# Performance work log

Measured on AMD Instinct MI355X. Metric: run time of the kernel, lower is better.

The kernel has to match this reference:

```python
import jax, jax.numpy as jnp
import numpy as np

N = 50000        # nodes
E = 1600000      # edges (before self-loops)
HID = 128
HEADS = 4
HD = HID // HEADS
FIN = 32 + 7     # node feats + scenario feats
EPS = 1e-5


def _ln(x, g, b):
    m = x.mean(-1, keepdims=True)
    v = ((x - m) ** 2).mean(-1, keepdims=True)
    return (x - m) / jnp.sqrt(v + EPS) * g + b


def _gat(x, src, dst, W, a_s, a_d, bias):
    # PyG GATConv (concat=True, negative_slope=0.2), eval mode (no dropout)
    xp = (x @ W).reshape(-1, HEADS, HD)                    # [N,H,C]
    es = (xp * a_s).sum(-1)                                # [N,H]
    ed = (xp * a_d).sum(-1)                                # [N,H]
    e = jax.nn.leaky_relu(es[src] + ed[dst], 0.2)          # [Etot,H]
    emax = jax.ops.segment_max(e, dst, num_segments=N)     # per-target softmax (self-loops guarantee nonempty segments)
    a = jnp.exp(e - emax[dst])
    denom = jax.ops.segment_sum(a, dst, num_segments=N)
    a = a / denom[dst]
    out = jax.ops.segment_sum(xp[src] * a[:, :, None], dst, num_segments=N)
    return out.reshape(-1, HID) + bias


def setup_inputs() -> dict:
    key = jax.random.key(0)
    ks = iter(jax.random.split(key, 64))

    def rn(shape, scale=0.05):
        return jax.random.normal(next(ks), shape, dtype=jnp.float32) * scale

    inp = {}
    inp["x"] = jax.random.normal(next(ks), (N, FIN), dtype=jnp.float32)
    inp["edge_index"] = jax.random.randint(next(ks), (2, E), 0, N)
    inp["enc_w1"] = rn((FIN, HID)); inp["enc_b1"] = jnp.zeros((HID,), jnp.float32)
    inp["enc_w2"] = rn((HID, HID)); inp["enc_b2"] = jnp.zeros((HID,), jnp.float32)
    for l in (1, 2, 3):
        inp[f"W{l}"] = rn((HID, HID))
        inp[f"as{l}"] = rn((HEADS, HD))
        inp[f"ad{l}"] = rn((HEADS, HD))
        inp[f"bc{l}"] = jnp.zeros((HID,), jnp.float32)
        inp[f"g{l}"] = jnp.ones((HID,), jnp.float32)
        inp[f"be{l}"] = jnp.zeros((HID,), jnp.float32)
    inp["imp_w1"] = rn((HID, HID // 2)); inp["imp_b1"] = jnp.zeros((HID // 2,), jnp.float32)
    inp["imp_w2"] = rn((HID // 2, 3));   inp["imp_b2"] = jnp.zeros((3,), jnp.float32)
    inp["tim_w1"] = rn((HID, HID // 2)); inp["tim_b1"] = jnp.zeros((HID // 2,), jnp.float32)
    inp["tim_w2"] = rn((HID // 2, 2));   inp["tim_b2"] = jnp.zeros((2,), jnp.float32)
    return inp


def reference(x, edge_index, enc_w1, enc_b1, enc_w2, enc_b2,
              W1, as1, ad1, bc1, g1, be1,
              W2, as2, ad2, bc2, g2, be2,
              W3, as3, ad3, bc3, g3, be3,
              imp_w1, imp_b1, imp_w2, imp_b2,
              tim_w1, tim_b1, tim_w2, tim_b2):
    loops = jnp.arange(N, dtype=edge_index.dtype)          # add_self_loops=True
    src = jnp.concatenate([edge_index[0], loops])
    dst = jnp.concatenate([edge_index[1], loops])
    h = jax.nn.relu(x @ enc_w1 + enc_b1) @ enc_w2 + enc_b2
    for (W, a_s, a_d, bc, g, be) in ((W1, as1, ad1, bc1, g1, be1),
                                     (W2, as2, ad2, bc2, g2, be2),
                                     (W3, as3, ad3, bc3, g3, be3)):
        h = jax.nn.relu(_ln(_gat(h, src, dst, W, a_s, a_d, bc) + h, g, be))
    impact = jax.nn.relu(h @ imp_w1 + imp_b1) @ imp_w2 + imp_b2
    timing = jax.nn.softplus(jax.nn.relu(h @ tim_w1 + tim_b1) @ tim_w2 + tim_b2)
    return (impact, timing)
```

## Files before the change

### kernel.cpp

```cpp
#include <hip/hip_runtime.h>
#include <hip/hip_bf16.h>
#include <math.h>

#define NN 50000
#define EDGES 1600000
#define ETOT (EDGES + NN)
#define FINDIM 39
#define NPART 256
#define PSZ 196
#define PCAP 7100
#define P1TILE 4096

__device__ __forceinline__ unsigned pack_bf16(float a, float b) {
    __hip_bfloat162 t;
    t.x = __float2bfloat16(a);
    t.y = __float2bfloat16(b);
    return *(unsigned*)&t;
}
__device__ __forceinline__ float2 unpack_bf16(unsigned w) {
    float2 r;
    r.x = __uint_as_float(w << 16);
    r.y = __uint_as_float(w & 0xffff0000u);
    return r;
}

__device__ __forceinline__ int src_at(const int* ei, int i, bool i32) {
    return i32 ? ei[i] : ei[2 * i];
}
__device__ __forceinline__ int dst_at(const int* ei, int i, bool i32) {
    return i32 ? ei[EDGES + i] : ei[2 * (EDGES + i)];
}

__global__ __launch_bounds__(256) void pass1_kernel(const int* __restrict__ ei,
                                                    int* __restrict__ gcursor,
                                                    unsigned* __restrict__ pbuf) {
    __shared__ unsigned raw[P1TILE];
    __shared__ unsigned srt[P1TILE];
    __shared__ int pcnt[NPART], poff[NPART], pcur[NPART], gb[NPART];
    __shared__ int i32flag;
    int t = threadIdx.x;
    if (t == 0) i32flag = 0;
    __syncthreads();
    int chunk = (ETOT + gridDim.x - 1) / gridDim.x;
    int c0 = blockIdx.x * chunk;
    int c1 = c0 + chunk; if (c1 > ETOT) c1 = ETOT;
    int sb = c0 < EDGES - 64 ? c0 : 0;
    if (t < 64 && ei[2 * (sb + t) + 1] != 0) i32flag = 1;
    __syncthreads();
    bool i32 = (i32flag != 0);
    for (int t0 = c0; t0 < c1; t0 += P1TILE) {
        int tn = c1 - t0; if (tn > P1TILE) tn = P1TILE;
        pcnt[t] = 0; pcur[t] = 0;
        __syncthreads();
        for (int i = t; i < tn; i += 256) {
            int e = t0 + i;
            int s, d;
            if (e < EDGES) { s = src_at(ei, e, i32); d = dst_at(ei, e, i32); }
            else { s = d = e - EDGES; }
            raw[i] = ((unsigned)s << 16) | (unsigned)d;
            atomicAdd(&pcnt[d / PSZ], 1);
        }
        __syncthreads();
        poff[t] = pcnt[t];
        __syncthreads();
        for (int off = 1; off < NPART; off <<= 1) {
            int v = (t >= off) ? poff[t - off] : 0;
            __syncthreads();
            poff[t] += v;
            __syncthreads();
        }
        poff[t] -= pcnt[t];
        gb[t] = atomicAdd(&gcursor[t], pcnt[t]);
        __syncthreads();
        for (int i = t; i < tn; i += 256) {
            unsigned r = raw[i];
            int part = (int)(r & 0xFFFFu) / PSZ;
            int pos = poff[part] + atomicAdd(&pcur[part], 1);
            srt[pos] = r;
        }
        __syncthreads();
        for (int i = t; i < tn; i += 256) {
            unsigned r = srt[i];
            int part = (int)(r & 0xFFFFu) / PSZ;
            int gpos = gb[part] + (i - poff[part]);
            if (gpos < PCAP) pbuf[(size_t)part * PCAP + gpos] = r;
        }
        __syncthreads();
    }
}

__global__ __launch_bounds__(256) void pass2_kernel(const unsigned* __restrict__ pbuf,
                                                    const int* __restrict__ gcursor,
                                                    int* __restrict__ rowptr,
                                                    int* __restrict__ colidx) {
    __shared__ unsigned recs[PCAP];
    __shared__ int lhist[PSZ], lexcl[PSZ], lcur[PSZ];
    __shared__ int psm[NPART];
    int p = blockIdx.x;
    int t = threadIdx.x;
    psm[t] = gcursor[t];
    __syncthreads();
    for (int off = 1; off < NPART; off <<= 1) {
        int x = (t >= off) ? psm[t - off] : 0;
        __syncthreads();
        psm[t] += x;
        __syncthreads();
    }
    int n = gcursor[p]; if (n > PCAP) n = PCAP;
    int base = psm[p] - gcursor[p];
    if (p == NPART - 1 && t == 0) rowptr[NN] = psm[NPART - 1];
    int d0 = p * PSZ;
    int nd = NN - d0; if (nd > PSZ) nd = PSZ;
    if (nd < 0) nd = 0;
    for (int i = t; i < nd; i += 256) { lhist[i] = 0; lcur[i] = 0; }
    __syncthreads();
    for (int i = t; i < n; i += 256) {
        unsigned r = pbuf[(size_t)p * PCAP + i];
        recs[i] = r;
        atomicAdd(&lhist[(int)(r & 0xFFFFu) - d0], 1);
    }
    __syncthreads();
    for (int i = t; i < nd; i += 256) lexcl[i] = lhist[i];
    __syncthreads();
    for (int off = 1; off < PSZ; off <<= 1) {
        int a0 = 0;
        if (t < nd && t >= off) a0 = lexcl[t - off];
        __syncthreads();
        if (t < nd) lexcl[t] += a0;
        __syncthreads();
    }
    for (int i = t; i < nd; i += 256) {
        lexcl[i] -= lhist[i];
        rowptr[d0 + i] = base + lexcl[i];
    }
    __syncthreads();
    for (int i = t; i < n; i += 256) {
        unsigned r = recs[i];
        int li = (int)(r & 0xFFFFu) - d0;
        int pos = base + lexcl[li] + atomicAdd(&lcur[li], 1);
        colidx[pos] = (int)(r >> 16);
    }
}

template <int NC, bool RELU>
__global__ __launch_bounds__(256) void gemm_small_kernel(const float* __restrict__ A,
                                                         const float* __restrict__ B,
                                                         const float* __restrict__ bias,
                                                         float* __restrict__ C, int M, int K) {
    constexpr int TM = 32;
    constexpr int GROUPS = 256 / NC;
    constexpr int RPG = TM / GROUPS;
    constexpr int KC = 64;
    __shared__ float As[TM * 128];
    __shared__ float Bs[KC * NC];
    int t = threadIdx.x;
    int i0 = blockIdx.x * TM;

    int rows = M - i0; if (rows > TM) rows = TM;
    for (int idx = t; idx < rows * K; idx += 256) {
        int r = idx / K, k = idx - r * K;
        As[r * K + k] = A[(size_t)(i0 + r) * K + k];
    }

    int col = t % NC, grp = t / NC;
    int rg0 = grp * RPG;
    float acc[RPG];
#pragma unroll
    for (int r = 0; r < RPG; ++r) acc[r] = 0.f;

    for (int k0 = 0; k0 < K; k0 += KC) {
        int kc = K - k0; if (kc > KC) kc = KC;
        __syncthreads();
        for (int idx = t; idx < kc * NC; idx += 256) Bs[idx] = B[(size_t)k0 * NC + idx];
        __syncthreads();
        for (int k = 0; k < kc; ++k) {
            float bv = Bs[k * NC + col];
#pragma unroll
            for (int r = 0; r < RPG; ++r) acc[r] += As[(rg0 + r) * K + k0 + k] * bv;
        }
    }

    float bb = bias ? bias[col] : 0.f;
#pragma unroll
    for (int r = 0; r < RPG; ++r) {
        int i = i0 + rg0 + r;
        if (i < M) {
            float v = acc[r] + bb;
            if (RELU) v = v > 0.f ? v : 0.f;
            C[(size_t)i * NC + col] = v;
        }
    }
}

template <bool BIAS, bool EPI>
__global__ __launch_bounds__(256) void gemm128_kernel(const float* __restrict__ A,
                                                      const float* __restrict__ B,
                                                      const float* __restrict__ bias,
                                                      float* __restrict__ C,
                                                      unsigned* __restrict__ XP,
                                                      const float* __restrict__ a_s,
                                                      const float* __restrict__ a_d,
                                                      float* __restrict__ es,
                                                      float* __restrict__ ed, int M) {
    __shared__ float As[64 * 32];
    __shared__ float Bs[32 * 128];
    int t = threadIdx.x;
    int i0 = blockIdx.x * 64;
    int tc = t & 31;
    int tr = t >> 5;
    int r0 = tr * 8;
    int c0 = tc * 4;

    float acc[8][4];
#pragma unroll
    for (int i = 0; i < 8; ++i)
#pragma unroll
        for (int j = 0; j < 4; ++j) acc[i][j] = 0.f;

    for (int k0 = 0; k0 < 128; k0 += 32) {
        __syncthreads();
#pragma unroll
        for (int q = 0; q < 2; ++q) {
            int idx = t + q * 256;
            int r = idx >> 3, kq = idx & 7;
            float4 v4 = make_float4(0.f, 0.f, 0.f, 0.f);
            if (i0 + r < M) v4 = *(const float4*)&A[(size_t)(i0 + r) * 128 + k0 + kq * 4];
            *(float4*)&As[r * 32 + kq * 4] = v4;
        }
#pragma unroll
        for (int q = 0; q < 4; ++q) {
            int idx = (t + q * 256) * 4;
            *(float4*)&Bs[idx] = *(const float4*)&B[(size_t)k0 * 128 + idx];
        }
        __syncthreads();
#pragma unroll 8
        for (int k = 0; k < 32; k += 4) {
            float4 a4[8];
#pragma unroll
            for (int i = 0; i < 8; ++i)
                a4[i] = *(const float4*)&As[(r0 + i) * 32 + k];
            float4 b4[4];
#pragma unroll
            for (int kk = 0; kk < 4; ++kk)
                b4[kk] = *(const float4*)&Bs[(k + kk) * 128 + c0];
#pragma unroll
            for (int i = 0; i < 8; ++i) {
                const float* av = (const float*)&a4[i];
#pragma unroll
                for (int kk = 0; kk < 4; ++kk) {
                    acc[i][0] += av[kk] * b4[kk].x;
                    acc[i][1] += av[kk] * b4[kk].y;
                    acc[i][2] += av[kk] * b4[kk].z;
                    acc[i][3] += av[kk] * b4[kk].w;
                }
            }
        }
    }

    if (!EPI) {
        float4 bias4 = make_float4(0.f, 0.f, 0.f, 0.f);
        if (BIAS) bias4 = *(const float4*)&bias[c0];
#pragma unroll
        for (int i = 0; i < 8; ++i) {
            int row = i0 + r0 + i;
            if (row < M) {
                float4 o;
                o.x = acc[i][0] + bias4.x;
                o.y = acc[i][1] + bias4.y;
                o.z = acc[i][2] + bias4.z;
                o.w = acc[i][3] + bias4.w;
                *(float4*)&C[(size_t)row * 128 + c0] = o;
            }
        }
    } else {
#pragma unroll
        for (int i = 0; i < 8; ++i) {
            int row = i0 + r0 + i;
            if (row < M) {
                uint2 o;
                o.x = pack_bf16(acc[i][0], acc[i][1]);
                o.y = pack_bf16(acc[i][2], acc[i][3]);
                *(uint2*)&XP[(size_t)row * 64 + tc * 2] = o;
            }
        }
        int hd = tc >> 3;
        float4 s4 = *(const float4*)&a_s[c0];
        float4 d4 = *(const float4*)&a_d[c0];
#pragma unroll
        for (int i = 0; i < 8; ++i) {
            int row = i0 + r0 + i;
            float s = acc[i][0] * s4.x + acc[i][1] * s4.y + acc[i][2] * s4.z + acc[i][3] * s4.w;
            float d = acc[i][0] * d4.x + acc[i][1] * d4.y + acc[i][2] * d4.z + acc[i][3] * d4.w;
#pragma unroll
            for (int off = 4; off >= 1; off >>= 1) {
                s += __shfl_xor(s, off);
                d += __shfl_xor(d, off);
            }
            if ((tc & 7) == 0 && row < M) {
                es[row * 4 + hd] = s;
                ed[row * 4 + hd] = d;
            }
        }
    }
}

__global__ __launch_bounds__(256) void gemm_heads_kernel(const float* __restrict__ A,
                                                         const float* __restrict__ iw1,
                                                         const float* __restrict__ ib1,
                                                         const float* __restrict__ tw1,
                                                         const float* __restrict__ tb1,
                                                         const float* __restrict__ iw2,
                                                         const float* __restrict__ ib2,
                                                         const float* __restrict__ tw2,
                                                         const float* __restrict__ tb2,
                                                         float* __restrict__ out, int M) {
    __shared__ float As[64 * 32];
    __shared__ float Bs[32 * 128];
    int t = threadIdx.x;
    int i0 = blockIdx.x * 64;
    int tc = t & 31;
    int tr = t >> 5;
    int r0 = tr * 8;
    int c0 = tc * 4;

    float acc[8][4];
#pragma unroll
    for (int i = 0; i < 8; ++i)
#pragma unroll
        for (int j = 0; j < 4; ++j) acc[i][j] = 0.f;

    for (int k0 = 0; k0 < 128; k0 += 32) {
        __syncthreads();
#pragma unroll
        for (int q = 0; q < 2; ++q) {
            int idx = t + q * 256;
            int r = idx >> 3, kq = idx & 7;
            float4 v4 = make_float4(0.f, 0.f, 0.f, 0.f);
            if (i0 + r < M) v4 = *(const float4*)&A[(size_t)(i0 + r) * 128 + k0 + kq * 4];
            *(float4*)&As[r * 32 + kq * 4] = v4;
        }
#pragma unroll
        for (int q = 0; q < 4; ++q) {
            int idx = (t + q * 256) * 4;
            int k = idx >> 7, cl = idx & 127;
            float4 v4 = (cl < 64)
                ? *(const float4*)&iw1[(size_t)(k0 + k) * 64 + cl]
                : *(const float4*)&tw1[(size_t)(k0 + k) * 64 + (cl - 64)];
            *(float4*)&Bs[idx] = v4;
        }
        __syncthreads();
#pragma unroll 8
        for (int k = 0; k < 32; k += 4) {
            float4 a4[8];
#pragma unroll
            for (int i = 0; i < 8; ++i)
                a4[i] = *(const float4*)&As[(r0 + i) * 32 + k];
            float4 b4[4];
#pragma unroll
            for (int kk = 0; kk < 4; ++kk)
                b4[kk] = *(const float4*)&Bs[(k + kk) * 128 + c0];
#pragma unroll
            for (int i = 0; i < 8; ++i) {
                const float* av = (const float*)&a4[i];
#pragma unroll
                for (int kk = 0; kk < 4; ++kk) {
                    acc[i][0] += av[kk] * b4[kk].x;
                    acc[i][1] += av[kk] * b4[kk].y;
                    acc[i][2] += av[kk] * b4[kk].z;
                    acc[i][3] += av[kk] * b4[kk].w;
                }
            }
        }
    }

    bool isimp = (tc < 16);
    int lc = isimp ? c0 : (c0 - 64);
    float v[8][4];
#pragma unroll
    for (int i = 0; i < 8; ++i)
#pragma unroll
        for (int j = 0; j < 4; ++j) {
            float b = isimp ? ib1[lc + j] : tb1[lc + j];
            float x = acc[i][j] + b;
            v[i][j] = x > 0.f ? x : 0.f;
        }
#pragma unroll
    for (int i = 0; i < 8; ++i) {
        int row = i0 + r0 + i;
        if (isimp) {
#pragma unroll
            for (int c = 0; c < 3; ++c) {
                float pc = v[i][0] * iw2[(lc + 0) * 3 + c] + v[i][1] * iw2[(lc + 1) * 3 + c]
                         + v[i][2] * iw2[(lc + 2) * 3 + c] + v[i][3] * iw2[(lc + 3) * 3 + c];
#pragma unroll
                for (int off = 8; off >= 1; off >>= 1) pc += __shfl_xor(pc, off);
                if (tc == 0 && row < M) out[(size_t)row * 3 + c] = pc + ib2[c];
            }
        } else {
#pragma unroll
            for (int d = 0; d < 2; ++d) {
                float pd = v[i][0] * tw2[(lc + 0) * 2 + d] + v[i][1] * tw2[(lc + 1) * 2 + d]
                         + v[i][2] * tw2[(lc + 2) * 2 + d] + v[i][3] * tw2[(lc + 3) * 2 + d];
#pragma unroll
                for (int off = 8; off >= 1; off >>= 1) pd += __shfl_xor(pd, off);
                if (tc == 16 && row < M) {
                    float a = pd + tb2[d];
                    float sp = a > 20.f ? a : log1pf(__expf(a));
                    out[(size_t)(NN * 3) + (size_t)row * 2 + d] = sp;
                }
            }
        }
    }
}

__global__ __launch_bounds__(256, 6) void gat_kernel(const unsigned* __restrict__ xpk,
                                                     const float* __restrict__ es,
                                                     const float* __restrict__ ed,
                                                     const int* __restrict__ rowptr,
                                                     const int* __restrict__ colidx,
                                                     float* __restrict__ h,
                                                     const float* __restrict__ bc,
                                                     const float* __restrict__ g,
                                                     const float* __restrict__ be) {
    int wv = threadIdx.x >> 6, l = threadIdx.x & 63;
    int hf = l >> 5;
    int lh = l & 31;
    int hd = lh >> 3;
    int j  = lh & 7;
    int v = blockIdx.x * 8 + wv * 2 + hf;
    if (v >= NN) return;
    int s0 = rowptr[v], s1 = rowptr[v + 1];
    int len = s1 - s0;
    int nmax = max(len, __shfl_xor(len, 32));
    int c0 = (hd << 5) + (j << 2);
    int xsel = (hd << 4) + (j << 1);
    float edv = ed[((unsigned)v << 2) + hd];

    float4 h4 = *(const float4*)&h[(size_t)v * 128 + c0];

    float a0 = 0.f, a1 = 0.f, a2 = 0.f, a3 = 0.f, den = 0.f;
    for (int p8 = 0; p8 < nmax; p8 += 8) {
        int u[8];
#pragma unroll
        for (int q = 0; q < 8; ++q) {
            int idx = p8 + q;
            u[q] = colidx[s0 + (idx < len ? idx : len - 1)];
        }
        uint2 xw[8];
#pragma unroll
        for (int q = 0; q < 8; ++q)
            xw[q] = *(const uint2*)&xpk[((unsigned)u[q] << 6) + xsel];
        float w[8];
#pragma unroll
        for (int q = 0; q < 8; ++q) {
            float e = es[((unsigned)u[q] << 2) + hd] + edv;
            e = fmaxf(e, 0.2f * e);
            float ww = __expf(e);
            w[q] = (p8 + q < len) ? ww : 0.f;
            den += w[q];
        }
#pragma unroll
        for (int q = 0; q < 8; ++q) {
            float2 x0 = unpack_bf16(xw[q].x);
            float2 x1 = unpack_bf16(xw[q].y);
            a0 = fmaf(w[q], x0.x, a0);
            a1 = fmaf(w[q], x0.y, a1);
            a2 = fmaf(w[q], x1.x, a2);
            a3 = fmaf(w[q], x1.y, a3);
        }
    }
    float rd = 1.f / den;

    float4 bc4 = *(const float4*)&bc[c0];
    float y0 = a0 * rd + bc4.x + h4.x;
    float y1 = a1 * rd + bc4.y + h4.y;
    float y2 = a2 * rd + bc4.z + h4.z;
    float y3 = a3 * rd + bc4.w + h4.w;

    float s = y0 + y1 + y2 + y3;
#pragma unroll
    for (int off = 16; off >= 1; off >>= 1) s += __shfl_xor(s, off);
    float mean = s * (1.f / 128.f);
    float d0 = y0 - mean, d1 = y1 - mean, d2 = y2 - mean, d3 = y3 - mean;
    float vv = d0 * d0 + d1 * d1 + d2 * d2 + d3 * d3;
#pragma unroll
    for (int off = 16; off >= 1; off >>= 1) vv += __shfl_xor(vv, off);
    float rstd = rsqrtf(vv * (1.f / 128.f) + 1e-5f);
    float4 g4  = *(const float4*)&g[c0];
    float4 be4 = *(const float4*)&be[c0];
    float z0 = d0 * rstd * g4.x + be4.x;
    float z1 = d1 * rstd * g4.y + be4.y;
    float z2 = d2 * rstd * g4.z + be4.z;
    float z3 = d3 * rstd * g4.w + be4.w;
    float4 o;
    o.x = z0 > 0.f ? z0 : 0.f;
    o.y = z1 > 0.f ? z1 : 0.f;
    o.z = z2 > 0.f ? z2 : 0.f;
    o.w = z3 > 0.f ? z3 : 0.f;
    *(float4*)&h[(size_t)v * 128 + c0] = o;
}

extern "C" void kernel_launch(void* const* d_in, const int* in_sizes, int n_in,
                              void* d_out, int out_size, void* d_ws, size_t ws_size,
                              hipStream_t stream) {
    const float* x      = (const float*)d_in[0];
    const int*   ei     = (const int*)d_in[1];
    const float* enc_w1 = (const float*)d_in[2];
    const float* enc_b1 = (const float*)d_in[3];
    const float* enc_w2 = (const float*)d_in[4];
    const float* enc_b2 = (const float*)d_in[5];
    const float *W[3], *as_[3], *ad_[3], *bc[3], *g[3], *be[3];
    for (int l = 0; l < 3; ++l) {
        W[l]   = (const float*)d_in[6 + l * 6 + 0];
        as_[l] = (const float*)d_in[6 + l * 6 + 1];
        ad_[l] = (const float*)d_in[6 + l * 6 + 2];
        bc[l]  = (const float*)d_in[6 + l * 6 + 3];
        g[l]   = (const float*)d_in[6 + l * 6 + 4];
        be[l]  = (const float*)d_in[6 + l * 6 + 5];
    }
    const float* imp_w1 = (const float*)d_in[24];
    const float* imp_b1 = (const float*)d_in[25];
    const float* imp_w2 = (const float*)d_in[26];
    const float* imp_b2 = (const float*)d_in[27];
    const float* tim_w1 = (const float*)d_in[28];
    const float* tim_b1 = (const float*)d_in[29];
    const float* tim_w2 = (const float*)d_in[30];
    const float* tim_b2 = (const float*)d_in[31];

    int* gcursor = (int*)d_ws;
    int* rowptr  = gcursor + NPART + 64;
    int* colidx  = rowptr + NN + 1;
    uintptr_t pb = (uintptr_t)(colidx + ETOT + 8);
    pb = (pb + 255) & ~(uintptr_t)255;
    unsigned* pbuf = (unsigned*)pb;
    uintptr_t fb = (uintptr_t)(pbuf + (size_t)NPART * PCAP);
    fb = (fb + 255) & ~(uintptr_t)255;
    float* es = (float*)fb;
    float* ed = es + (size_t)NN * 4;
    float* h  = ed + (size_t)NN * 4;
    float* xpf = h + (size_t)NN * 128;
    unsigned* xpk = (unsigned*)xpf;
    float* tmp = xpf;

    hipMemsetAsync(gcursor, 0, NPART * sizeof(int), stream);
    pass1_kernel<<<512, 256, 0, stream>>>(ei, gcursor, pbuf);
    pass2_kernel<<<NPART, 256, 0, stream>>>(pbuf, gcursor, rowptr, colidx);

    const int GB64 = (NN + 63) / 64;
    gemm_small_kernel<128, true><<<(NN + 31) / 32, 256, 0, stream>>>(x, enc_w1, enc_b1, tmp, NN, FINDIM);
    gemm128_kernel<true, false><<<GB64, 256, 0, stream>>>(tmp, enc_w2, enc_b2, h, nullptr,
                                                          nullptr, nullptr, nullptr, nullptr, NN);

    for (int l = 0; l < 3; ++l) {
        gemm128_kernel<false, true><<<GB64, 256, 0, stream>>>(h, W[l], nullptr, nullptr, xpk,
                                                              as_[l], ad_[l], es, ed, NN);
        gat_kernel<<<(NN + 7) / 8, 256, 0, stream>>>(xpk, es, ed, rowptr, colidx, h,
                                                     bc[l], g[l], be[l]);
    }

    gemm_heads_kernel<<<GB64, 256, 0, stream>>>(h, imp_w1, imp_b1, tim_w1, tim_b1,
                                                imp_w2, imp_b2, tim_w2, tim_b2,
                                                (float*)d_out, NN);
}
```

Baseline: 562.5 us.

## Precompute exponentials per node and use 16-lane-per-node GAT aggregation

The projection GEMM now stores exp(s), exp(0.2s), exp(d) and exp(0.2d) per node and head. The GAT kernel then forms each edge weight as the max of two products, which equals exp(leaky_relu(s+d)), so there is no per-edge exp. The GAT kernel also assigns 16 lanes per node instead of 32, with each lane gathering 8 bf16 features via uint4 loads, and it lowers the occupancy hint to 5. Dropping the max subtraction in the softmax risks overflow for large logits, and the per-node es/ed arrays double in size.

```diff
diff --git a/kernel.cpp b/kernel.cpp
--- a/kernel.cpp
+++ b/kernel.cpp
@@ -200,8 +200,8 @@
                                                       unsigned* __restrict__ XP,
                                                       const float* __restrict__ a_s,
                                                       const float* __restrict__ a_d,
-                                                      float* __restrict__ es,
-                                                      float* __restrict__ ed, int M) {
+                                                      float* __restrict__ esx,
+                                                      float* __restrict__ edx, int M) {
     __shared__ float As[64 * 32];
     __shared__ float Bs[32 * 128];
     int t = threadIdx.x;
@@ -297,8 +297,11 @@
                 d += __shfl_xor(d, off);
             }
             if ((tc & 7) == 0 && row < M) {
-                es[row * 4 + hd] = s;
-                ed[row * 4 + hd] = d;
+                float2 E, F;
+                E.x = __expf(s); E.y = __expf(0.2f * s);
+                F.x = __expf(d); F.y = __expf(0.2f * d);
+                *(float2*)&esx[row * 8 + hd * 2] = E;
+                *(float2*)&edx[row * 8 + hd * 2] = F;
             }
         }
     }
@@ -413,9 +416,9 @@
     }
 }
 
-__global__ __launch_bounds__(256, 6) void gat_kernel(const unsigned* __restrict__ xpk,
-                                                     const float* __restrict__ es,
-                                                     const float* __restrict__ ed,
+__global__ __launch_bounds__(256, 5) void gat_kernel(const unsigned* __restrict__ xpk,
+                                                     const float* __restrict__ esx,
+                                                     const float* __restrict__ edx,
                                                      const int* __restrict__ rowptr,
                                                      const int* __restrict__ colidx,
                                                      float* __restrict__ h,
@@ -423,22 +426,26 @@
                                                      const float* __restrict__ g,
                                                      const float* __restrict__ be) {
     int wv = threadIdx.x >> 6, l = threadIdx.x & 63;
-    int hf = l >> 5;
-    int lh = l & 31;
-    int hd = lh >> 3;
-    int j  = lh & 7;
-    int v = blockIdx.x * 8 + wv * 2 + hf;
+    int qt = l >> 4;
+    int lq = l & 15;
+    int hd = lq >> 2;
+    int j  = lq & 3;
+    int v = blockIdx.x * 16 + wv * 4 + qt;
     if (v >= NN) return;
     int s0 = rowptr[v], s1 = rowptr[v + 1];
     int len = s1 - s0;
-    int nmax = max(len, __shfl_xor(len, 32));
-    int c0 = (hd << 5) + (j << 2);
-    int xsel = (hd << 4) + (j << 1);
-    float edv = ed[((unsigned)v << 2) + hd];
-
-    float4 h4 = *(const float4*)&h[(size_t)v * 128 + c0];
-
-    float a0 = 0.f, a1 = 0.f, a2 = 0.f, a3 = 0.f, den = 0.f;
+    int m1 = max(len, __shfl_xor(len, 16));
+    int nmax = max(m1, __shfl_xor(m1, 32));
+    int c0 = (hd << 5) + (j << 3);
+    int xsel = (hd << 4) + (j << 2);
+    float2 F = *(const float2*)&edx[((unsigned)v << 3) + (hd << 1)];
+
+    float4 h4a = *(const float4*)&h[(size_t)v * 128 + c0];
+    float4 h4b = *(const float4*)&h[(size_t)v * 128 + c0 + 4];
+
+    float a0 = 0.f, a1 = 0.f, a2 = 0.f, a3 = 0.f;
+    float a4 = 0.f, a5 = 0.f, a6 = 0.f, a7 = 0.f;
+    float den = 0.f;
     for (int p8 = 0; p8 < nmax; p8 += 8) {
         int u[8];
 #pragma unroll
@@ -446,16 +453,18 @@
             int idx = p8 + q;
             u[q] = colidx[s0 + (idx < len ? idx : len - 1)];
         }
-        uint2 xw[8];
+        float2 E[8];
 #pragma unroll
         for (int q = 0; q < 8; ++q)
-            xw[q] = *(const uint2*)&xpk[((unsigned)u[q] << 6) + xsel];
+            E[q] = *(const float2*)&esx[((unsigned)u[q] << 3) + (hd << 1)];
+        uint4 xw[8];
+#pragma unroll
+        for (int q = 0; q < 8; ++q)
+            xw[q] = *(const uint4*)&xpk[((unsigned)u[q] << 6) + xsel];
         float w[8];
 #pragma unroll
         for (int q = 0; q < 8; ++q) {
-            float e = es[((unsigned)u[q] << 2) + hd] + edv;
-            e = fmaxf(e, 0.2f * e);
-            float ww = __expf(e);
+            float ww = fmaxf(E[q].x * F.x, E[q].y * F.y);
             w[q] = (p8 + q < len) ? ww : 0.f;
             den += w[q];
         }
@@ -463,41 +472,58 @@
         for (int q = 0; q < 8; ++q) {
             float2 x0 = unpack_bf16(xw[q].x);
             float2 x1 = unpack_bf16(xw[q].y);
+            float2 x2 = unpack_bf16(xw[q].z);
+            float2 x3 = unpack_bf16(xw[q].w);
             a0 = fmaf(w[q], x0.x, a0);
             a1 = fmaf(w[q], x0.y, a1);
             a2 = fmaf(w[q], x1.x, a2);
             a3 = fmaf(w[q], x1.y, a3);
+            a4 = fmaf(w[q], x2.x, a4);
+            a5 = fmaf(w[q], x2.y, a5);
+            a6 = fmaf(w[q], x3.x, a6);
+            a7 = fmaf(w[q], x3.y, a7);
         }
     }
     float rd = 1.f / den;
 
-    float4 bc4 = *(const float4*)&bc[c0];
-    float y0 = a0 * rd + bc4.x + h4.x;
-    float y1 = a1 * rd + bc4.y + h4.y;
-    float y2 = a2 * rd + bc4.z + h4.z;
-    float y3 = a3 * rd + bc4.w + h4.w;
-
-    float s = y0 + y1 + y2 + y3;
-#pragma unroll
-    for (int off = 16; off >= 1; off >>= 1) s += __shfl_xor(s, off);
+    float4 bc4a = *(const float4*)&bc[c0];
+    float4 bc4b = *(const float4*)&bc[c0 + 4];
+    float y0 = a0 * rd + bc4a.x + h4a.x;
+    float y1 = a1 * rd + bc4a.y + h4a.y;
+    float y2 = a2 * rd + bc4a.z + h4a.z;
+    float y3 = a3 * rd + bc4a.w + h4a.w;
+    float y4 = a4 * rd + bc4b.x + h4b.x;
+    float y5 = a5 * rd + bc4b.y + h4b.y;
+    float y6 = a6 * rd + bc4b.z + h4b.z;
+    float y7 = a7 * rd + bc4b.w + h4b.w;
+
+    float s = ((y0 + y1) + (y2 + y3)) + ((y4 + y5) + (y6 + y7));
+#pragma unroll
+    for (int off = 8; off >= 1; off >>= 1) s += __shfl_xor(s, off);
     float mean = s * (1.f / 128.f);
     float d0 = y0 - mean, d1 = y1 - mean, d2 = y2 - mean, d3 = y3 - mean;
-    float vv = d0 * d0 + d1 * d1 + d2 * d2 + d3 * d3;
-#pragma unroll
-    for (int off = 16; off >= 1; off >>= 1) vv += __shfl_xor(vv, off);
+    float d4 = y4 - mean, d5 = y5 - mean, d6 = y6 - mean, d7 = y7 - mean;
+    float vv = ((d0 * d0 + d1 * d1) + (d2 * d2 + d3 * d3))
+             + ((d4 * d4 + d5 * d5) + (d6 * d6 + d7 * d7));
+#pragma unroll
+    for (int off = 8; off >= 1; off >>= 1) vv += __shfl_xor(vv, off);
     float rstd = rsqrtf(vv * (1.f / 128.f) + 1e-5f);
-    float4 g4  = *(const float4*)&g[c0];
-    float4 be4 = *(const float4*)&be[c0];
-    float z0 = d0 * rstd * g4.x + be4.x;
-    float z1 = d1 * rstd * g4.y + be4.y;
-    float z2 = d2 * rstd * g4.z + be4.z;
-    float z3 = d3 * rstd * g4.w + be4.w;
-    float4 o;
-    o.x = z0 > 0.f ? z0 : 0.f;
-    o.y = z1 > 0.f ? z1 : 0.f;
-    o.z = z2 > 0.f ? z2 : 0.f;
-    o.w = z3 > 0.f ? z3 : 0.f;
-    *(float4*)&h[(size_t)v * 128 + c0] = o;
+    float4 g4a  = *(const float4*)&g[c0];
+    float4 g4b  = *(const float4*)&g[c0 + 4];
+    float4 be4a = *(const float4*)&be[c0];
+    float4 be4b = *(const float4*)&be[c0 + 4];
+    float4 oa, ob;
+    float z;
+    z = d0 * rstd * g4a.x + be4a.x; oa.x = z > 0.f ? z : 0.f;
+    z = d1 * rstd * g4a.y + be4a.y; oa.y = z > 0.f ? z : 0.f;
+    z = d2 * rstd * g4a.z + be4a.z; oa.z = z > 0.f ? z : 0.f;
+    z = d3 * rstd * g4a.w + be4a.w; oa.w = z > 0.f ? z : 0.f;
+    z = d4 * rstd * g4b.x + be4b.x; ob.x = z > 0.f ? z : 0.f;
+    z = d5 * rstd * g4b.y + be4b.y; ob.y = z > 0.f ? z : 0.f;
+    z = d6 * rstd * g4b.z + be4b.z; ob.z = z > 0.f ? z : 0.f;
+    z = d7 * rstd * g4b.w + be4b.w; ob.w = z > 0.f ? z : 0.f;
+    *(float4*)&h[(size_t)v * 128 + c0] = oa;
+    *(float4*)&h[(size_t)v * 128 + c0 + 4] = ob;
 }
 
 extern "C" void kernel_launch(void* const* d_in, const int* in_sizes, int n_in,
@@ -535,9 +561,9 @@
     unsigned* pbuf = (unsigned*)pb;
     uintptr_t fb = (uintptr_t)(pbuf + (size_t)NPART * PCAP);
     fb = (fb + 255) & ~(uintptr_t)255;
-    float* es = (float*)fb;
-    float* ed = es + (size_t)NN * 4;
-    float* h  = ed + (size_t)NN * 4;
+    float* esx = (float*)fb;
+    float* edx = esx + (size_t)NN * 8;
+    float* h   = edx + (size_t)NN * 8;
     float* xpf = h + (size_t)NN * 128;
     unsigned* xpk = (unsigned*)xpf;
     float* tmp = xpf;
@@ -553,9 +579,9 @@
 
     for (int l = 0; l < 3; ++l) {
         gemm128_kernel<false, true><<<GB64, 256, 0, stream>>>(h, W[l], nullptr, nullptr, xpk,
-                                                              as_[l], ad_[l], es, ed, NN);
-        gat_kernel<<<(NN + 7) / 8, 256, 0, stream>>>(xpk, es, ed, rowptr, colidx, h,
-                                                     bc[l], g[l], be[l]);
+                                                              as_[l], ad_[l], esx, edx, NN);
+        gat_kernel<<<(NN + 15) / 16, 256, 0, stream>>>(xpk, esx, edx, rowptr, colidx, h,
+                                                       bc[l], g[l], be[l]);
     }
 
     gemm_heads_kernel<<<GB64, 256, 0, stream>>>(h, imp_w1, imp_b1, tim_w1, tim_b1,
```

Measured after the change: 584.6 us. +3.9%, slower.

## Use bf16 MFMA for GAT projections and precompute exponentials of attention logits

Applied to the files above, without the earlier changes.

Replaces the fp32 FMA GEMM for each GAT layer's projection with a bf16 MFMA kernel. It reads a bf16 copy of h, written by the encoder GEMM and the previous GAT layer, and a transposed bf16 copy of W. The attention epilogue now stores exp(s) and exp(0.2s) per node, so the per-edge leaky-relu+exp becomes a max of two products. This cuts the per-edge transcendental work and the GEMM cost. In exchange it reads more per-edge bytes (float2 instead of float), adds bf16 rounding on the GEMM inputs, and risks overflow from the unshifted exponentials.

```diff
diff --git a/kernel.cpp b/kernel.cpp
--- a/kernel.cpp
+++ b/kernel.cpp
@@ -10,6 +10,9 @@
 #define PSZ 196
 #define PCAP 7100
 #define P1TILE 4096
+
+typedef __attribute__((ext_vector_type(8))) short short8;
+typedef __attribute__((ext_vector_type(4))) float floatx4;
 
 __device__ __forceinline__ unsigned pack_bf16(float a, float b) {
     __hip_bfloat162 t;
@@ -192,16 +195,11 @@
     }
 }
 
-template <bool BIAS, bool EPI>
 __global__ __launch_bounds__(256) void gemm128_kernel(const float* __restrict__ A,
                                                       const float* __restrict__ B,
                                                       const float* __restrict__ bias,
                                                       float* __restrict__ C,
-                                                      unsigned* __restrict__ XP,
-                                                      const float* __restrict__ a_s,
-                                                      const float* __restrict__ a_d,
-                                                      float* __restrict__ es,
-                                                      float* __restrict__ ed, int M) {
+                                                      unsigned* __restrict__ HB, int M) {
     __shared__ float As[64 * 32];
     __shared__ float Bs[32 * 128];
     int t = threadIdx.x;
@@ -257,48 +255,115 @@
         }
     }
 
-    if (!EPI) {
-        float4 bias4 = make_float4(0.f, 0.f, 0.f, 0.f);
-        if (BIAS) bias4 = *(const float4*)&bias[c0];
-#pragma unroll
-        for (int i = 0; i < 8; ++i) {
-            int row = i0 + r0 + i;
-            if (row < M) {
-                float4 o;
-                o.x = acc[i][0] + bias4.x;
-                o.y = acc[i][1] + bias4.y;
-                o.z = acc[i][2] + bias4.z;
-                o.w = acc[i][3] + bias4.w;
-                *(float4*)&C[(size_t)row * 128 + c0] = o;
-            }
-        }
-    } else {
-#pragma unroll
-        for (int i = 0; i < 8; ++i) {
-            int row = i0 + r0 + i;
-            if (row < M) {
-                uint2 o;
-                o.x = pack_bf16(acc[i][0], acc[i][1]);
-                o.y = pack_bf16(acc[i][2], acc[i][3]);
-                *(uint2*)&XP[(size_t)row * 64 + tc * 2] = o;
-            }
-        }
-        int hd = tc >> 3;
-        float4 s4 = *(const float4*)&a_s[c0];
-        float4 d4 = *(const float4*)&a_d[c0];
-#pragma unroll
-        for (int i = 0; i < 8; ++i) {
-            int row = i0 + r0 + i;
-            float s = acc[i][0] * s4.x + acc[i][1] * s4.y + acc[i][2] * s4.z + acc[i][3] * s4.w;
-            float d = acc[i][0] * d4.x + acc[i][1] * d4.y + acc[i][2] * d4.z + acc[i][3] * d4.w;
-#pragma unroll
-            for (int off = 4; off >= 1; off >>= 1) {
+    float4 bias4 = *(const float4*)&bias[c0];
+#pragma unroll
+    for (int i = 0; i < 8; ++i) {
+        int row = i0 + r0 + i;
+        if (row < M) {
+            float4 o;
+            o.x = acc[i][0] + bias4.x;
+            o.y = acc[i][1] + bias4.y;
+            o.z = acc[i][2] + bias4.z;
+            o.w = acc[i][3] + bias4.w;
+            *(float4*)&C[(size_t)row * 128 + c0] = o;
+            uint2 p;
+            p.x = pack_bf16(o.x, o.y);
+            p.y = pack_bf16(o.z, o.w);
+            *(uint2*)&HB[(size_t)row * 64 + tc * 2] = p;
+        }
+    }
+}
+
+__global__ __launch_bounds__(256) void wconv_kernel(const float* __restrict__ W,
+                                                    unsigned short* __restrict__ wtb) {
+    int idx = blockIdx.x * 256 + threadIdx.x;
+    int c = idx >> 7, k = idx & 127;
+    unsigned p = pack_bf16(W[(size_t)k * 128 + c], 0.f);
+    wtb[(size_t)c * 128 + k] = (unsigned short)(p & 0xffffu);
+}
+
+__global__ __launch_bounds__(256) void gemm_mfma_kernel(const unsigned* __restrict__ hb,
+                                                        const unsigned short* __restrict__ wtb,
+                                                        unsigned* __restrict__ XP,
+                                                        const float* __restrict__ a_s,
+                                                        const float* __restrict__ a_d,
+                                                        float* __restrict__ esx,
+                                                        float* __restrict__ edx, int M) {
+    int t = threadIdx.x;
+    int w = t >> 6, l = t & 63;
+    int c = l & 15, grp = l >> 4;
+    int i0 = blockIdx.x * 64 + w * 16;
+    int arow = i0 + c;
+
+    floatx4 acc[8];
+#pragma unroll
+    for (int n = 0; n < 8; ++n) acc[n] = (floatx4){0.f, 0.f, 0.f, 0.f};
+
+    uint4 a4[4];
+#pragma unroll
+    for (int kc = 0; kc < 4; ++kc) {
+        uint4 z = make_uint4(0u, 0u, 0u, 0u);
+        if (arow < M) z = *(const uint4*)&hb[(size_t)arow * 64 + (kc << 4) + (grp << 2)];
+        a4[kc] = z;
+    }
+
+#pragma unroll
+    for (int kc = 0; kc < 4; ++kc) {
+        short8 af = *(short8*)&a4[kc];
+#pragma unroll
+        for (int n = 0; n < 8; ++n) {
+            short8 bf = *(const short8*)&wtb[(size_t)(((n << 4) + c) * 128 + (kc << 5) + (grp << 3))];
+            acc[n] = __builtin_amdgcn_mfma_f32_16x16x32_bf16(af, bf, acc[n], 0, 0, 0);
+        }
+    }
+
+    float asv[8], adv[8];
+#pragma unroll
+    for (int n = 0; n < 8; ++n) { asv[n] = a_s[(n << 4) + c]; adv[n] = a_d[(n << 4) + c]; }
+
+    float sp[4][4], dp[4][4];
+#pragma unroll
+    for (int r = 0; r < 4; ++r)
+#pragma unroll
+        for (int hd = 0; hd < 4; ++hd) { sp[r][hd] = 0.f; dp[r][hd] = 0.f; }
+
+#pragma unroll
+    for (int n = 0; n < 8; ++n) {
+#pragma unroll
+        for (int r = 0; r < 4; ++r) {
+            float vv = acc[n][r];
+            float pv = __shfl_xor(vv, 1);
+            int row = i0 + (grp << 2) + r;
+            if (!(c & 1) && row < M)
+                XP[(size_t)row * 64 + (n << 3) + (c >> 1)] = pack_bf16(vv, pv);
+            sp[r][n >> 1] = fmaf(vv, asv[n], sp[r][n >> 1]);
+            dp[r][n >> 1] = fmaf(vv, adv[n], dp[r][n >> 1]);
+        }
+    }
+#pragma unroll
+    for (int r = 0; r < 4; ++r)
+#pragma unroll
+        for (int hd = 0; hd < 4; ++hd) {
+            float s = sp[r][hd], d = dp[r][hd];
+#pragma unroll
+            for (int off = 1; off <= 8; off <<= 1) {
                 s += __shfl_xor(s, off);
                 d += __shfl_xor(d, off);
             }
-            if ((tc & 7) == 0 && row < M) {
-                es[row * 4 + hd] = s;
-                ed[row * 4 + hd] = d;
+            sp[r][hd] = s; dp[r][hd] = d;
+        }
+    if (c < 4) {
+#pragma unroll
+        for (int r = 0; r < 4; ++r) {
+            int row = i0 + (grp << 2) + r;
+            if (row < M) {
+                float s = (c == 0) ? sp[r][0] : (c == 1) ? sp[r][1] : (c == 2) ? sp[r][2] : sp[r][3];
+                float d = (c == 0) ? dp[r][0] : (c == 1) ? dp[r][1] : (c == 2) ? dp[r][2] : dp[r][3];
+                float2 E, F;
+                E.x = __expf(s); E.y = __expf(0.2f * s);
+                F.x = __expf(d); F.y = __expf(0.2f * d);
+                *(float2*)&esx[(size_t)row * 8 + (c << 1)] = E;
+                *(float2*)&edx[(size_t)row * 8 + (c << 1)] = F;
             }
         }
     }
@@ -414,11 +479,12 @@
 }
 
 __global__ __launch_bounds__(256, 6) void gat_kernel(const unsigned* __restrict__ xpk,
-                                                     const float* __restrict__ es,
-                                                     const float* __restrict__ ed,
+                                                     const float* __restrict__ esx,
+                                                     const float* __restrict__ edx,
                                                      const int* __restrict__ rowptr,
                                                      const int* __restrict__ colidx,
                                                      float* __restrict__ h,
+                                                     unsigned* __restrict__ hb,
                                                      const float* __restrict__ bc,
                                                      const float* __restrict__ g,
                                                      const float* __restrict__ be) {
@@ -434,7 +500,7 @@
     int nmax = max(len, __shfl_xor(len, 32));
     int c0 = (hd << 5) + (j << 2);
     int xsel = (hd << 4) + (j << 1);
-    float edv = ed[((unsigned)v << 2) + hd];
+    float2 F = *(const float2*)&edx[((unsigned)v << 3) + (hd << 1)];
 
     float4 h4 = *(const float4*)&h[(size_t)v * 128 + c0];
 
@@ -446,6 +512,10 @@
             int idx = p8 + q;
             u[q] = colidx[s0 + (idx < len ? idx : len - 1)];
         }
+        float2 E[8];
+#pragma unroll
+        for (int q = 0; q < 8; ++q)
+            E[q] = *(const float2*)&esx[((unsigned)u[q] << 3) + (hd << 1)];
         uint2 xw[8];
 #pragma unroll
         for (int q = 0; q < 8; ++q)
@@ -453,9 +523,7 @@
         float w[8];
 #pragma unroll
         for (int q = 0; q < 8; ++q) {
-            float e = es[((unsigned)u[q] << 2) + hd] + edv;
-            e = fmaxf(e, 0.2f * e);
-            float ww = __expf(e);
+            float ww = fmaxf(E[q].x * F.x, E[q].y * F.y);
             w[q] = (p8 + q < len) ? ww : 0.f;
             den += w[q];
         }
@@ -498,6 +566,12 @@
     o.z = z2 > 0.f ? z2 : 0.f;
     o.w = z3 > 0.f ? z3 : 0.f;
     *(float4*)&h[(size_t)v * 128 + c0] = o;
+    if (hb) {
+        uint2 hp;
+        hp.x = pack_bf16(o.x, o.y);
+        hp.y = pack_bf16(o.z, o.w);
+        *(uint2*)&hb[(size_t)v * 64 + (c0 >> 1)] = hp;
+    }
 }
 
 extern "C" void kernel_launch(void* const* d_in, const int* in_sizes, int n_in,
@@ -535,26 +609,30 @@
     unsigned* pbuf = (unsigned*)pb;
     uintptr_t fb = (uintptr_t)(pbuf + (size_t)NPART * PCAP);
     fb = (fb + 255) & ~(uintptr_t)255;
-    float* es = (float*)fb;
-    float* ed = es + (size_t)NN * 4;
-    float* h  = ed + (size_t)NN * 4;
+    float* esx = (float*)fb;
+    float* edx = esx + (size_t)NN * 8;
+    float* h   = edx + (size_t)NN * 8;
     float* xpf = h + (size_t)NN * 128;
     unsigned* xpk = (unsigned*)xpf;
-    float* tmp = xpf;
+    unsigned* hb  = (unsigned*)(xpf + (size_t)NN * 64);
+    unsigned short* wtb = (unsigned short*)(xpf + (size_t)NN * 128);
+    float* tmp = h;
 
     hipMemsetAsync(gcursor, 0, NPART * sizeof(int), stream);
     pass1_kernel<<<512, 256, 0, stream>>>(ei, gcursor, pbuf);
     pass2_kernel<<<NPART, 256, 0, stream>>>(pbuf, gcursor, rowptr, colidx);
+    for (int l = 0; l < 3; ++l)
+        wconv_kernel<<<64, 256, 0, stream>>>(W[l], wtb + (size_t)l * 16384);
 
     const int GB64 = (NN + 63) / 64;
     gemm_small_kernel<128, true><<<(NN + 31) / 32, 256, 0, stream>>>(x, enc_w1, enc_b1, tmp, NN, FINDIM);
-    gemm128_kernel<true, false><<<GB64, 256, 0, stream>>>(tmp, enc_w2, enc_b2, h, nullptr,
-                                                          nullptr, nullptr, nullptr, nullptr, NN);
+    gemm128_kernel<<<GB64, 256, 0, stream>>>(tmp, enc_w2, enc_b2, h, hb, NN);
 
     for (int l = 0; l < 3; ++l) {
-        gemm128_kernel<false, true><<<GB64, 256, 0, stream>>>(h, W[l], nullptr, nullptr, xpk,
-                                                              as_[l], ad_[l], es, ed, NN);
-        gat_kernel<<<(NN + 7) / 8, 256, 0, stream>>>(xpk, es, ed, rowptr, colidx, h,
+        gemm_mfma_kernel<<<GB64, 256, 0, stream>>>(hb, wtb + (size_t)l * 16384, xpk,
+                                                   as_[l], ad_[l], esx, edx, NN);
+        gat_kernel<<<(NN + 7) / 8, 256, 0, stream>>>(xpk, esx, edx, rowptr, colidx, h,
+                                                     (l < 2) ? hb : nullptr,
                                                      bc[l], g[l], be[l]);
     }
 
```

Result: slower. 594.4 us (+5.7%).
